# Optimization experiments

Measured on AMD Instinct MI355X. Metric: run time of the kernel, lower is better.

Reference implementation:

```python
import jax, jax.numpy as jnp
import numpy as np

EMBED_DIM = 512
HEADS = 8
ATTN_DIM = EMBED_DIM // HEADS
PF_DIM = 2048
B, L = 4, 2048
LN_EPS = 1e-5


def _linear(x, W, b):
    # nn.Linear: x @ W.T + b, W is [out, in]
    return jnp.einsum('bld,od->blo', x, W) + b


def _layer_norm(x, g, b):
    mu = jnp.mean(x, axis=-1, keepdims=True)
    var = jnp.mean(jnp.square(x - mu), axis=-1, keepdims=True)
    return (x - mu) * jax.lax.rsqrt(var + LN_EPS) * g + b


def _qkv(src, Wq, bq, Wk, bk, Wv, bv):
    def split(t):
        Bb, Ll, _ = t.shape
        return t.reshape(Bb, Ll, HEADS, ATTN_DIM).transpose(0, 2, 1, 3)  # [B,H,L,Dh]
    return (split(_linear(src, Wq, bq)),
            split(_linear(src, Wk, bk)),
            split(_linear(src, Wv, bv)))


def _attention(inp, Q, K1, K2, V1, V2, Wo, bo, ln_g, ln_b, W1, b1, W2, b2):
    # non-softmax linear attention: (Q K1^T) V1 + (Q K2^T) V2
    attn = (jnp.einsum('bhqk,bhkd->bhqd', jnp.einsum('bhqd,bhkd->bhqk', Q, K1), V1)
            + jnp.einsum('bhqk,bhkd->bhqd', jnp.einsum('bhqd,bhkd->bhqk', Q, K2), V2))
    Bb = Q.shape[0]
    attn = attn.transpose(0, 2, 1, 3).reshape(Bb, -1, HEADS * ATTN_DIM)  # [B,L,D]
    x = _linear(attn, Wo, bo)
    x = _layer_norm(inp + x, ln_g, ln_b)          # dropout p=0 (eval)
    ff = _linear(jax.nn.relu(_linear(x, W1, b1)), W2, b2)
    x = _layer_norm(x + ff, ln_g, ln_b)
    return x


def setup_inputs() -> dict:
    key = jax.random.key(0)
    ks = jax.random.split(key, 16)
    s = 0.02
    return {
        'question': jax.random.normal(ks[0], (B, L, EMBED_DIM), jnp.float32),
        'query': jax.random.normal(ks[1], (B, L, EMBED_DIM), jnp.float32),
        'Wq': jax.random.normal(ks[2], (EMBED_DIM, EMBED_DIM), jnp.float32) * s,
        'bq': jnp.zeros((EMBED_DIM,), jnp.float32),
        'Wk': jax.random.normal(ks[3], (EMBED_DIM, EMBED_DIM), jnp.float32) * s,
        'bk': jnp.zeros((EMBED_DIM,), jnp.float32),
        'Wv': jax.random.normal(ks[4], (EMBED_DIM, EMBED_DIM), jnp.float32) * s,
        'bv': jnp.zeros((EMBED_DIM,), jnp.float32),
        'Wo': jax.random.normal(ks[5], (EMBED_DIM, EMBED_DIM), jnp.float32) * s,
        'bo': jnp.zeros((EMBED_DIM,), jnp.float32),
        'ln_g': jnp.ones((EMBED_DIM,), jnp.float32),
        'ln_b': jnp.zeros((EMBED_DIM,), jnp.float32),
        'W1': jax.random.normal(ks[6], (PF_DIM, EMBED_DIM), jnp.float32) * s,
        'b1': jnp.zeros((PF_DIM,), jnp.float32),
        'W2': jax.random.normal(ks[7], (EMBED_DIM, PF_DIM), jnp.float32) * s,
        'b2': jnp.zeros((EMBED_DIM,), jnp.float32),
    }


def reference(question, query, Wq, bq, Wk, bk, Wv, bv, Wo, bo, ln_g, ln_b, W1, b1, W2, b2):
    Q1, K1, V1 = _qkv(question, Wq, bq, Wk, bk, Wv, bv)
    Q2, K2, V2 = _qkv(query, Wq, bq, Wk, bk, Wv, bv)
    question_attn = _attention(question, Q1, K1, K2, V1, V2, Wo, bo, ln_g, ln_b, W1, b1, W2, b2)
    query_attn = _attention(query, Q2, K2, K1, V2, V1, Wo, bo, ln_g, ln_b, W1, b1, W2, b2)
    return jnp.concatenate([question_attn, query_attn], axis=-1)
```

## Files before the change

### kernel.cpp

```cpp
#include <hip/hip_runtime.h>
#include <stdint.h>


#define Bq 4
#define Lq 2048
#define Dq 512
#define PFq 2048
#define Mrows 16384
#define MiBu 1048576ull
#define NSLICE 16

typedef __attribute__((ext_vector_type(8))) short frag_ab;
typedef __attribute__((ext_vector_type(4))) float frag_cd;
typedef __attribute__((ext_vector_type(8))) unsigned short ushort8v;

__device__ __forceinline__ unsigned short f2b(float f) {
    union { float f; uint32_t u; } x; x.f = f;
    uint32_t r = x.u + 0x7fffu + ((x.u >> 16) & 1u);
    return (unsigned short)(r >> 16);
}
__device__ __forceinline__ float b2f(unsigned short u) {
    union { uint32_t u; float f; } x; x.u = ((uint32_t)u) << 16;
    return x.f;
}

#define GLD16(g, l)                                                              \
    __builtin_amdgcn_global_load_lds(                                            \
        (const __attribute__((address_space(1))) void*)(const void*)(g),         \
        (__attribute__((address_space(3))) void*)(void*)(l), 16, 0, 0)

#define STG(BUFOFS, REGOFS, GB, ROWOFS, TILE, KS)                                \
    { GLD16((GB) + (size_t)(ROWOFS) * (KS) + (TILE) * 64,                        \
            Sh + (BUFOFS) + (REGOFS) + ld);                                      \
      GLD16((GB) + ((size_t)(ROWOFS) + 64) * (KS) + (TILE) * 64,                 \
            Sh + (BUFOFS) + (REGOFS) + ld + 4096); }

#define VMW(N) asm volatile("s_waitcnt vmcnt(" #N ")" ::: "memory")

#define PHASE(CB, M0, LOADB, STAGE_STMT, WAIT_STMT)                              \
    {                                                                            \
        frag_ab a00 = *(const frag_ab*)&Sh[(CB) + (wm + (M0)*16 + lr) * 64 + xo0];      \
        frag_ab a01 = *(const frag_ab*)&Sh[(CB) + (wm + (M0)*16 + lr) * 64 + xo1];      \
        frag_ab a10 = *(const frag_ab*)&Sh[(CB) + (wm + (M0)*16 + 16 + lr) * 64 + xo0]; \
        frag_ab a11 = *(const frag_ab*)&Sh[(CB) + (wm + (M0)*16 + 16 + lr) * 64 + xo1]; \
        if (LOADB) {                                                             \
            _Pragma("unroll")                                                    \
            for (int j = 0; j < 4; ++j) {                                        \
                bf[j][0] = *(const frag_ab*)&Sh[(CB) + 16384 + (wn + j*16 + lr)*64 + xo0]; \
                bf[j][1] = *(const frag_ab*)&Sh[(CB) + 16384 + (wn + j*16 + lr)*64 + xo1]; \
            }                                                                    \
        }                                                                        \
        STAGE_STMT;                                                              \
        WAIT_STMT;                                                               \
        __builtin_amdgcn_sched_barrier(0);                                       \
        __builtin_amdgcn_s_barrier();                                            \
        asm volatile("s_waitcnt lgkmcnt(0)" ::: "memory");                       \
        __builtin_amdgcn_sched_barrier(0);                                       \
        __builtin_amdgcn_s_setprio(1);                                           \
        _Pragma("unroll")                                                        \
        for (int j = 0; j < 4; ++j) {                                            \
            acc[(M0)][j]   = __builtin_amdgcn_mfma_f32_16x16x32_bf16(a00, bf[j][0], acc[(M0)][j], 0,0,0);   \
            acc[(M0)][j]   = __builtin_amdgcn_mfma_f32_16x16x32_bf16(a01, bf[j][1], acc[(M0)][j], 0,0,0);   \
            acc[(M0)+1][j] = __builtin_amdgcn_mfma_f32_16x16x32_bf16(a10, bf[j][0], acc[(M0)+1][j], 0,0,0); \
            acc[(M0)+1][j] = __builtin_amdgcn_mfma_f32_16x16x32_bf16(a11, bf[j][1], acc[(M0)+1][j], 0,0,0); \
        }                                                                        \
        __builtin_amdgcn_s_setprio(0);                                           \
        __builtin_amdgcn_sched_barrier(0);                                       \
        __builtin_amdgcn_s_barrier();                                            \
        __builtin_amdgcn_sched_barrier(0);                                       \
    }

__global__ __launch_bounds__(512, 2) void gemm_256(
    const unsigned short* __restrict__ A, const unsigned short* __restrict__ Wt,
    const float* __restrict__ bias, unsigned short* __restrict__ outB,
    int M, int N, int relu)
{
    __shared__ __align__(16) unsigned short Sh[65536];
    const int tid = threadIdx.x;
    const int lane = tid & 63;
    const int w = tid >> 6;
    const int wm = (w >> 2) * 128;
    const int wn = (w & 3) * 64;
    const int lr = lane & 15;
    const int quad = lane >> 4;
    const int xo0 = ((quad ^ (lr & 7)) << 3);
    const int xo1 = (((4 | quad) ^ (lr & 7)) << 3);

    const int b0 = blockIdx.x;
    const int xcd = b0 & 7, slot = b0 >> 3;
    const int mloc = (M >> 8) >> 3;
    const size_t bm = (size_t)(xcd * mloc + slot % mloc) * 256;
    const size_t bn = (size_t)(slot / mloc) * 256;

    const int ar = tid >> 3;
    const int sw = ((tid & 7) ^ (ar & 7)) << 3;
    const unsigned short* Ag = A  + (bm + ar) * (size_t)512 + sw;
    const unsigned short* Bg = Wt + (bn + ar) * (size_t)512 + sw;
    const int ld = tid * 8;

    frag_cd acc[8][4] = {};
    frag_ab bf[4][2];

    STG(0,     16384, Bg, 0,   0, 512);
    STG(0,     24576, Bg, 128, 0, 512);
    STG(0,     0,     Ag, 0,   0, 512);
    STG(0,     8192,  Ag, 128, 0, 512);
    STG(32768, 16384, Bg, 0,   1, 512);
    STG(32768, 24576, Bg, 128, 1, 512);
    VMW(4);
    __builtin_amdgcn_sched_barrier(0);
    __builtin_amdgcn_s_barrier();
    __builtin_amdgcn_sched_barrier(0);

    for (int I = 0; I < 3; ++I) {
        const int tb = 2 * I + 1, tc = 2 * I + 2, td = 2 * I + 3;
        PHASE(0,     0, 1, STG(32768, 0,     Ag, 0,   tb, 512), (void)0);
        PHASE(0,     2, 0, STG(32768, 8192,  Ag, 128, tb, 512), (void)0);
        PHASE(0,     4, 0, STG(0,     16384, Bg, 0,   tc, 512), (void)0);
        PHASE(0,     6, 0, STG(0,     24576, Bg, 128, tc, 512), VMW(4));
        PHASE(32768, 0, 1, STG(0,     0,     Ag, 0,   tc, 512), (void)0);
        PHASE(32768, 2, 0, STG(0,     8192,  Ag, 128, tc, 512), (void)0);
        PHASE(32768, 4, 0, STG(32768, 16384, Bg, 0,   td, 512), (void)0);
        PHASE(32768, 6, 0, STG(32768, 24576, Bg, 128, td, 512), VMW(4));
    }
    PHASE(0,     0, 1, STG(32768, 0,    Ag, 0,   7, 512), (void)0);
    PHASE(0,     2, 0, STG(32768, 8192, Ag, 128, 7, 512), (void)0);
    PHASE(0,     4, 0, (void)0, (void)0);
    PHASE(0,     6, 0, (void)0, VMW(0));
    PHASE(32768, 0, 1, (void)0, (void)0);
    PHASE(32768, 2, 0, (void)0, (void)0);
    PHASE(32768, 4, 0, (void)0, (void)0);
    PHASE(32768, 6, 0, (void)0, (void)0);

    float bv[4];
#pragma unroll
    for (int j = 0; j < 4; ++j) bv[j] = bias[(int)bn + wn + j * 16 + lr];
    unsigned short* Cs = Sh + w * 8192;
#pragma unroll
    for (int m = 0; m < 8; ++m)
#pragma unroll
        for (int j = 0; j < 4; ++j)
#pragma unroll
            for (int r = 0; r < 4; ++r) {
                float v = acc[m][j][r] + bv[j];
                if (relu) v = fmaxf(v, 0.f);
                Cs[(m * 16 + quad * 4 + r) * 64 + j * 16 + lr] = f2b(v);
            }
    const int rl = lane >> 3, c8 = (lane & 7) * 8;
#pragma unroll
    for (int k = 0; k < 16; ++k) {
        const int row = rl + k * 8;
        ushort8v val = *(const ushort8v*)&Cs[row * 64 + c8];
        *(ushort8v*)(outB + (size_t)(bm + wm + row) * N + bn + wn + c8) = val;
    }
}

__global__ __launch_bounds__(512, 2) void gemm_n128(
    const unsigned short* __restrict__ A, const unsigned short* __restrict__ Wt,
    const float* __restrict__ bias,
    const float* __restrict__ resA, const float* __restrict__ resB,
    unsigned short* __restrict__ outB, int N, int K, int mode)
{
    __shared__ __align__(16) unsigned short Sh[49152];
    const int tid = threadIdx.x;
    const int lane = tid & 63;
    const int w = tid >> 6;
    const int wm = (w >> 1) * 64;
    const int wn = (w & 1) * 64;
    const int lr = lane & 15;
    const int quad = lane >> 4;
    const int xo0 = ((quad ^ (lr & 7)) << 3);
    const int xo1 = (((4 | quad) ^ (lr & 7)) << 3);

    const int b0 = blockIdx.x;
    const int xcd = b0 & 7, slot = b0 >> 3;
    const size_t bm = (size_t)(xcd * 8 + (slot & 7)) * 256;
    const size_t bn = (size_t)(slot >> 3) * 128;

    const int ar = tid >> 3;
    const int sw = ((tid & 7) ^ (ar & 7)) << 3;
    const unsigned short* Ag = A  + (bm + ar) * (size_t)K + sw;
    const unsigned short* Bg = Wt + (bn + ar) * (size_t)K + sw;
    const int ld = tid * 8;

    frag_cd acc[4][4] = {};
    frag_ab bf[4][2];

    STG(0,     16384, Bg, 0,   0, K);
    STG(0,     0,     Ag, 0,   0, K);
    STG(0,     8192,  Ag, 128, 0, K);
    STG(24576, 16384, Bg, 0,   1, K);
    VMW(2);
    __builtin_amdgcn_sched_barrier(0);
    __builtin_amdgcn_s_barrier();
    __builtin_amdgcn_sched_barrier(0);

    const int nIter = K >> 7;
    for (int I = 0; I < nIter - 1; ++I) {
        const int tb = 2 * I + 1, tc = 2 * I + 2, td = 2 * I + 3;
        PHASE(0,     0, 1, { STG(24576, 0, Ag, 0, tb, K); STG(24576, 8192, Ag, 128, tb, K); }, (void)0);
        PHASE(0,     2, 0, STG(0, 16384, Bg, 0, tc, K), VMW(2));
        PHASE(24576, 0, 1, { STG(0, 0, Ag, 0, tc, K); STG(0, 8192, Ag, 128, tc, K); }, (void)0);
        PHASE(24576, 2, 0, STG(24576, 16384, Bg, 0, td, K), VMW(2));
    }
    {
        const int tb = (K >> 6) - 1;
        PHASE(0,     0, 1, { STG(24576, 0, Ag, 0, tb, K); STG(24576, 8192, Ag, 128, tb, K); }, (void)0);
        PHASE(0,     2, 0, (void)0, VMW(0));
        PHASE(24576, 0, 1, (void)0, (void)0);
        PHASE(24576, 2, 0, (void)0, (void)0);
    }

    float bv[4];
#pragma unroll
    for (int j = 0; j < 4; ++j) bv[j] = bias[(int)bn + wn + j * 16 + lr];
    unsigned short* Cs = Sh + w * 4096;
#pragma unroll
    for (int m = 0; m < 4; ++m)
#pragma unroll
        for (int j = 0; j < 4; ++j)
#pragma unroll
            for (int r = 0; r < 4; ++r)
                Cs[(m * 16 + quad * 4 + r) * 64 + j * 16 + lr] = f2b(acc[m][j][r] + bv[j]);
    const int rl = lane >> 3, c8 = (lane & 7) * 8;
#pragma unroll
    for (int k = 0; k < 8; ++k) {
        const int row = rl + k * 8;
        const int grow = (int)bm + wm + row;
        const size_t idx = (size_t)grow * N + bn + wn + c8;
        ushort8v val = *(const ushort8v*)&Cs[row * 64 + c8];
        if (mode == 0) {
            *(ushort8v*)(outB + idx) = val;
            continue;
        }
        float vv[8];
#pragma unroll
        for (int t = 0; t < 8; ++t) vv[t] = b2f(val[t]);
        if (mode == 1) {
            const float* rp = (grow < 8192) ? resA + idx : resB + idx - (size_t)8192 * N;
            float4 ra = *(const float4*)(rp);
            float4 rb = *(const float4*)(rp + 4);
            vv[0] += ra.x; vv[1] += ra.y; vv[2] += ra.z; vv[3] += ra.w;
            vv[4] += rb.x; vv[5] += rb.y; vv[6] += rb.z; vv[7] += rb.w;
        } else {
            ushort8v old = *(const ushort8v*)(outB + idx);
#pragma unroll
            for (int t = 0; t < 8; ++t) vv[t] += b2f(old[t]);
        }
        ushort8v o;
#pragma unroll
        for (int t = 0; t < 8; ++t) o[t] = f2b(vv[t]);
        *(ushort8v*)(outB + idx) = o;
    }
}

__global__ __launch_bounds__(256) void convert_all(
    const float* __restrict__ Wq, const float* __restrict__ Wk,
    const float* __restrict__ Wv, const float* __restrict__ Wo,
    const float* __restrict__ W1, const float* __restrict__ W2,
    const float* __restrict__ question, const float* __restrict__ query,
    const float* __restrict__ bqp, const float* __restrict__ bkp,
    const float* __restrict__ bvp,
    unsigned short* __restrict__ Wqkvb, unsigned short* __restrict__ Wob,
    unsigned short* __restrict__ W1b, unsigned short* __restrict__ W2b,
    unsigned short* __restrict__ Xb, float* __restrict__ bqkv)
{
    const int b = blockIdx.x;
    const float* src; unsigned short* dst; size_t off;
    if (b < 256)        { src = Wq; dst = Wqkvb;          off = (size_t)b * 1024; }
    else if (b < 512)   { src = Wk; dst = Wqkvb + 262144; off = (size_t)(b - 256) * 1024; }
    else if (b < 768)   { src = Wv; dst = Wqkvb + 524288; off = (size_t)(b - 512) * 1024; }
    else if (b < 1024)  { src = Wo; dst = Wob;            off = (size_t)(b - 768) * 1024; }
    else if (b < 2048)  { src = W1; dst = W1b;            off = (size_t)(b - 1024) * 1024; }
    else if (b < 3072)  { src = W2; dst = W2b;            off = (size_t)(b - 2048) * 1024; }
    else if (b < 7168)  { src = question; dst = Xb;       off = (size_t)(b - 3072) * 1024; }
    else if (b < 11264) { src = query; dst = Xb + 4194304; off = (size_t)(b - 7168) * 1024; }
    else {
        const int n = (b - 11264) * 256 + threadIdx.x;
        bqkv[n] = (n < 512) ? bqp[n] : (n < 1024) ? bkp[n - 512] : bvp[n - 1024];
        return;
    }
    const size_t idx = off + threadIdx.x * 4;
    float4 v = *(const float4*)(src + idx);
    ushort4 o;
    o.x = f2b(v.x); o.y = f2b(v.y); o.z = f2b(v.z); o.w = f2b(v.w);
    *(ushort4*)(dst + idx) = o;
}

__global__ __launch_bounds__(256) void s_kernel(
    const unsigned short* __restrict__ QKV, float* __restrict__ Spart)
{
    const int bh = blockIdx.x;
    const int sl = blockIdx.y;
    const int b = bh >> 3, h = bh & 7;
    const int pass = sl >> 3;
    const int l0 = (sl & 7) * 256;
    __shared__ float Ks[64][64];
    __shared__ float Vs[64][64];
    const int tid = threadIdx.x;
    const int tx = tid & 15, ty = tid >> 4;
    const int srow = tid >> 3;
    const int scol = (tid & 7) * 8;
    const size_t rowbase = (size_t)pass * 8192 + (size_t)b * Lq + l0;

    float acc[4][4] = {};

    for (int t0 = 0; t0 < 256; t0 += 64) {
        const unsigned short* kp0 = QKV + (rowbase + t0 + srow) * 1536 + 512 + h * 64 + scol;
        const unsigned short* kp1 = kp0 + (size_t)32 * 1536;
        ushort8v k0 = *(const ushort8v*)kp0;
        ushort8v v0 = *(const ushort8v*)(kp0 + 512);
        ushort8v k1 = *(const ushort8v*)kp1;
        ushort8v v1 = *(const ushort8v*)(kp1 + 512);
        __syncthreads();
#pragma unroll
        for (int e = 0; e < 8; ++e) {
            Ks[srow][scol + e]      = b2f(k0[e]);
            Vs[srow][scol + e]      = b2f(v0[e]);
            Ks[srow + 32][scol + e] = b2f(k1[e]);
            Vs[srow + 32][scol + e] = b2f(v1[e]);
        }
        __syncthreads();
#pragma unroll 4
        for (int rr = 0; rr < 64; ++rr) {
            const float4 kf = *(const float4*)&Ks[rr][ty * 4];
            const float4 vf = *(const float4*)&Vs[rr][tx * 4];
            acc[0][0] = fmaf(kf.x, vf.x, acc[0][0]);
            acc[0][1] = fmaf(kf.x, vf.y, acc[0][1]);
            acc[0][2] = fmaf(kf.x, vf.z, acc[0][2]);
            acc[0][3] = fmaf(kf.x, vf.w, acc[0][3]);
            acc[1][0] = fmaf(kf.y, vf.x, acc[1][0]);
            acc[1][1] = fmaf(kf.y, vf.y, acc[1][1]);
            acc[1][2] = fmaf(kf.y, vf.z, acc[1][2]);
            acc[1][3] = fmaf(kf.y, vf.w, acc[1][3]);
            acc[2][0] = fmaf(kf.z, vf.x, acc[2][0]);
            acc[2][1] = fmaf(kf.z, vf.y, acc[2][1]);
            acc[2][2] = fmaf(kf.z, vf.z, acc[2][2]);
            acc[2][3] = fmaf(kf.z, vf.w, acc[2][3]);
            acc[3][0] = fmaf(kf.w, vf.x, acc[3][0]);
            acc[3][1] = fmaf(kf.w, vf.y, acc[3][1]);
            acc[3][2] = fmaf(kf.w, vf.z, acc[3][2]);
            acc[3][3] = fmaf(kf.w, vf.w, acc[3][3]);
        }
    }

    float* Sp = Spart + ((size_t)bh * NSLICE + sl) * 4096;
#pragma unroll
    for (int i = 0; i < 4; ++i) {
        float4 o = make_float4(acc[i][0], acc[i][1], acc[i][2], acc[i][3]);
        *(float4*)(Sp + (ty * 4 + i) * 64 + tx * 4) = o;
    }
}

__global__ __launch_bounds__(256) void sbt_convert(
    const float* __restrict__ Spart, unsigned short* __restrict__ Sbt)
{
    const int bh = blockIdx.x;
    const int uo = blockIdx.y;
    const float* Sp = Spart + (size_t)bh * (NSLICE * 4096);
    unsigned short* Dp = Sbt + (size_t)bh * 4096;
    const int t = threadIdx.x;
#pragma unroll
    for (int u = 0; u < 4; ++u) {
        const int d = (uo * 4 + u) * 256 + t;
        float v = 0.f;
#pragma unroll
        for (int s = 0; s < NSLICE; ++s) v += Sp[(size_t)s * 4096 + d];
        const int row = d >> 6, col = d & 63;
        Dp[(row >> 5) * 2048 + col * 32 + (row & 31)] = f2b(v);
    }
}

__global__ __launch_bounds__(256) void attn_mfma(
    const unsigned short* __restrict__ QKV, const unsigned short* __restrict__ Sbt,
    unsigned short* __restrict__ Ob)
{
    __shared__ __align__(16) unsigned short Sh[2 * 128 * 32 + 2 * 64 * 32];
    unsigned short* At = Sh;
    unsigned short* Bt = Sh + 2 * 128 * 32;
    const int h = blockIdx.x;
    const int rbase = blockIdx.y * 128;
    const int b = (rbase >> 11) & 3;
    const int bh = b * 8 + h;
    const int tid = threadIdx.x;
    const int lane = tid & 63;
    const int w = tid >> 6;
    const int lr = lane & 15;
    const int quad = lane >> 4;

    {
        const int rloc = tid >> 2, c8 = (tid & 3) * 8;
#pragma unroll
        for (int it = 0; it < 4; ++it) {
            const int kk = it & 1, rh = it >> 1;
            const unsigned short* g = QKV +
                ((size_t)rbase + rh * 64 + rloc) * 1536 + h * 64 + kk * 32 + c8;
            GLD16(g, At + kk * 4096 + rh * 2048 + w * 512);
        }
        const unsigned short* Sg = Sbt + (size_t)bh * 4096 + tid * 8;
#pragma unroll
        for (int bi = 0; bi < 2; ++bi)
            GLD16(Sg + bi * 2048, Bt + bi * 2048 + w * 512);
    }
    __syncthreads();

    frag_cd acc[2][4] = {};
#pragma unroll
    for (int kk = 0; kk < 2; ++kk) {
        frag_ab a[2], bfr[4];
#pragma unroll
        for (int i = 0; i < 2; ++i)
            a[i] = *(const frag_ab*)&At[kk * 4096 + (w * 32 + i * 16 + lr) * 32 + quad * 8];
#pragma unroll
        for (int j = 0; j < 4; ++j)
            bfr[j] = *(const frag_ab*)&Bt[kk * 2048 + (j * 16 + lr) * 32 + quad * 8];
#pragma unroll
        for (int i = 0; i < 2; ++i)
#pragma unroll
            for (int j = 0; j < 4; ++j)
                acc[i][j] = __builtin_amdgcn_mfma_f32_16x16x32_bf16(a[i], bfr[j], acc[i][j], 0, 0, 0);
    }

    __syncthreads();
    unsigned short* Cs = Sh + w * 2048;
#pragma unroll
    for (int i = 0; i < 2; ++i)
#pragma unroll
        for (int j = 0; j < 4; ++j)
#pragma unroll
            for (int r = 0; r < 4; ++r)
                Cs[(i * 16 + quad * 4 + r) * 64 + j * 16 + lr] = f2b(acc[i][j][r]);
    const int rl = lane >> 3;
    const int c8o = (lane & 7) * 8;
#pragma unroll
    for (int k = 0; k < 4; ++k) {
        const int row = rl + k * 8;
        ushort8v val = *(const ushort8v*)&Cs[row * 64 + c8o];
        *(ushort8v*)(Ob + (size_t)(rbase + w * 32 + row) * 512 + h * 64 + c8o) = val;
    }
}

__global__ __launch_bounds__(256) void ln_b16_inplace(
    unsigned short* __restrict__ Y, const float* __restrict__ g,
    const float* __restrict__ bta)
{
    __shared__ float part[8];
    const int row = blockIdx.x;
    const int t = threadIdx.x;
    const int w = t >> 6;
    unsigned short* yr = Y + (size_t)row * Dq;
    const float v0 = b2f(yr[t]), v1 = b2f(yr[t + 256]);
    float s = v0 + v1;
#pragma unroll
    for (int off = 32; off; off >>= 1) s += __shfl_xor(s, off, 64);
    if ((t & 63) == 0) part[w] = s;
    __syncthreads();
    const float mean = (part[0] + part[1] + part[2] + part[3]) * (1.f / Dq);
    const float d0 = v0 - mean, d1 = v1 - mean;
    float q = d0 * d0 + d1 * d1;
#pragma unroll
    for (int off = 32; off; off >>= 1) q += __shfl_xor(q, off, 64);
    if ((t & 63) == 0) part[4 + w] = q;
    __syncthreads();
    const float rstd = rsqrtf((part[4] + part[5] + part[6] + part[7]) * (1.f / Dq) + 1e-5f);
    yr[t] = f2b(d0 * rstd * g[t] + bta[t]);
    yr[t + 256] = f2b(d1 * rstd * g[t + 256] + bta[t + 256]);
}

__global__ __launch_bounds__(256) void ln_b16_out(
    const unsigned short* __restrict__ Y, const float* __restrict__ g,
    const float* __restrict__ bta, float* __restrict__ out)
{
    __shared__ float part[8];
    const int row = blockIdx.x;
    const int t = threadIdx.x;
    const int w = t >> 6;
    const unsigned short* yr = Y + (size_t)row * Dq;
    const float v0 = b2f(yr[t]), v1 = b2f(yr[t + 256]);
    float s = v0 + v1;
#pragma unroll
    for (int off = 32; off; off >>= 1) s += __shfl_xor(s, off, 64);
    if ((t & 63) == 0) part[w] = s;
    __syncthreads();
    const float mean = (part[0] + part[1] + part[2] + part[3]) * (1.f / Dq);
    const float d0 = v0 - mean, d1 = v1 - mean;
    float q = d0 * d0 + d1 * d1;
#pragma unroll
    for (int off = 32; off; off >>= 1) q += __shfl_xor(q, off, 64);
    if ((t & 63) == 0) part[4 + w] = q;
    __syncthreads();
    const float rstd = rsqrtf((part[4] + part[5] + part[6] + part[7]) * (1.f / Dq) + 1e-5f);
    const int half = row >> 13, br = row & 8191;
    float* orow = out + (size_t)br * 1024 + half * 512;
    orow[t] = d0 * rstd * g[t] + bta[t];
    orow[t + 256] = d1 * rstd * g[t + 256] + bta[t + 256];
}

extern "C" void kernel_launch(void* const* d_in, const int* in_sizes, int n_in,
                              void* d_out, int out_size, void* d_ws, size_t ws_size,
                              hipStream_t stream)
{
    const float* question = (const float*)d_in[0];
    const float* query    = (const float*)d_in[1];
    const float* Wq = (const float*)d_in[2];  const float* bqp = (const float*)d_in[3];
    const float* Wk = (const float*)d_in[4];  const float* bkp = (const float*)d_in[5];
    const float* Wv = (const float*)d_in[6];  const float* bvp = (const float*)d_in[7];
    const float* Wo = (const float*)d_in[8];  const float* bo  = (const float*)d_in[9];
    const float* ln_g = (const float*)d_in[10]; const float* ln_b = (const float*)d_in[11];
    const float* W1 = (const float*)d_in[12]; const float* b1 = (const float*)d_in[13];
    const float* W2 = (const float*)d_in[14]; const float* b2 = (const float*)d_in[15];
    float* out = (float*)d_out;
    char* ws = (char*)d_ws;

    unsigned short* QKVb  = (unsigned short*)(ws);
    unsigned short* attnb = (unsigned short*)(ws + 48 * MiBu);
    float* Spart          = (float*)(ws + 48 * MiBu);
    unsigned short* Xb    = (unsigned short*)(ws + 64 * MiBu);
    unsigned short* xbuf  = (unsigned short*)(ws + 64 * MiBu);
    unsigned short* hb    = (unsigned short*)(ws);
    char* wp = ws + 80 * MiBu + 524288;
    unsigned short* Wqkvb = (unsigned short*)wp;  wp += 1536 * 512 * 2;
    unsigned short* Wob   = (unsigned short*)wp;  wp += 512 * 512 * 2;
    unsigned short* W1b   = (unsigned short*)wp;  wp += 2048 * 512 * 2;
    unsigned short* W2b   = (unsigned short*)wp;  wp += 512 * 2048 * 2;
    unsigned short* Sbt   = (unsigned short*)wp;  wp += 32 * 4096 * 2;
    float* bqkv           = (float*)wp;

    dim3 blk(256);

    convert_all<<<11270, blk, 0, stream>>>(Wq, Wk, Wv, Wo, W1, W2, question, query,
                                           bqp, bkp, bvp,
                                           Wqkvb, Wob, W1b, W2b, Xb, bqkv);

    gemm_n128<<<dim3(768), dim3(512), 0, stream>>>(Xb, Wqkvb, bqkv,
                                                   nullptr, nullptr, QKVb,
                                                   1536, 512, 0);

    s_kernel<<<dim3(32, NSLICE), blk, 0, stream>>>(QKVb, Spart);
    sbt_convert<<<dim3(32, 4), blk, 0, stream>>>(Spart, Sbt);
    attn_mfma<<<dim3(8, 128), blk, 0, stream>>>(QKVb, Sbt, attnb);

    gemm_n128<<<dim3(256), dim3(512), 0, stream>>>(attnb, Wob, bo,
                                                   question, query, xbuf,
                                                   512, 512, 1);

    ln_b16_inplace<<<Mrows, blk, 0, stream>>>(xbuf, ln_g, ln_b);

    gemm_256<<<dim3(512), dim3(512), 0, stream>>>(xbuf, W1b, b1, hb,
                                                  Mrows, PFq, 1);

    gemm_n128<<<dim3(256), dim3(512), 0, stream>>>(hb, W2b, b2,
                                                   nullptr, nullptr, xbuf,
                                                   512, 2048, 2);

    ln_b16_out<<<Mrows, blk, 0, stream>>>(xbuf, ln_g, ln_b, out);
}
```

Before: 301.0 us.

## Unify GEMMs into triple-buffered 256x128 kernel with a deeper prefetch pipeline

Replaces the 256x256 FFN1 GEMM and the double-buffered 256x128 GEMM with one triple-buffered 256x128 kernel that keeps two K-tiles in flight. It generalises the M mapping and adds a ReLU flag, so FFN1 now runs on 1024 smaller tiles. The deeper prefetch is meant to hide global-load latency. In exchange it uses more LDS (144KB per block), which may reduce occupancy, and FFN1 loses the larger tile's data reuse.

```diff
diff --git a/kernel.cpp b/kernel.cpp
--- a/kernel.cpp
+++ b/kernel.cpp
@@ -30,9 +30,9 @@
         (__attribute__((address_space(3))) void*)(void*)(l), 16, 0, 0)
 
 #define STG(BUFOFS, REGOFS, GB, ROWOFS, TILE, KS)                                \
-    { GLD16((GB) + (size_t)(ROWOFS) * (KS) + (TILE) * 64,                        \
+    { GLD16((GB) + (size_t)(ROWOFS) * (KS) + (size_t)(TILE) * 64,                \
             Sh + (BUFOFS) + (REGOFS) + ld);                                      \
-      GLD16((GB) + ((size_t)(ROWOFS) + 64) * (KS) + (TILE) * 64,                 \
+      GLD16((GB) + ((size_t)(ROWOFS) + 64) * (KS) + (size_t)(TILE) * 64,         \
             Sh + (BUFOFS) + (REGOFS) + ld + 4096); }
 
 #define VMW(N) asm volatile("s_waitcnt vmcnt(" #N ")" ::: "memory")
@@ -70,98 +70,13 @@
         __builtin_amdgcn_sched_barrier(0);                                       \
     }
 
-__global__ __launch_bounds__(512, 2) void gemm_256(
-    const unsigned short* __restrict__ A, const unsigned short* __restrict__ Wt,
-    const float* __restrict__ bias, unsigned short* __restrict__ outB,
-    int M, int N, int relu)
-{
-    __shared__ __align__(16) unsigned short Sh[65536];
-    const int tid = threadIdx.x;
-    const int lane = tid & 63;
-    const int w = tid >> 6;
-    const int wm = (w >> 2) * 128;
-    const int wn = (w & 3) * 64;
-    const int lr = lane & 15;
-    const int quad = lane >> 4;
-    const int xo0 = ((quad ^ (lr & 7)) << 3);
-    const int xo1 = (((4 | quad) ^ (lr & 7)) << 3);
-
-    const int b0 = blockIdx.x;
-    const int xcd = b0 & 7, slot = b0 >> 3;
-    const int mloc = (M >> 8) >> 3;
-    const size_t bm = (size_t)(xcd * mloc + slot % mloc) * 256;
-    const size_t bn = (size_t)(slot / mloc) * 256;
-
-    const int ar = tid >> 3;
-    const int sw = ((tid & 7) ^ (ar & 7)) << 3;
-    const unsigned short* Ag = A  + (bm + ar) * (size_t)512 + sw;
-    const unsigned short* Bg = Wt + (bn + ar) * (size_t)512 + sw;
-    const int ld = tid * 8;
-
-    frag_cd acc[8][4] = {};
-    frag_ab bf[4][2];
-
-    STG(0,     16384, Bg, 0,   0, 512);
-    STG(0,     24576, Bg, 128, 0, 512);
-    STG(0,     0,     Ag, 0,   0, 512);
-    STG(0,     8192,  Ag, 128, 0, 512);
-    STG(32768, 16384, Bg, 0,   1, 512);
-    STG(32768, 24576, Bg, 128, 1, 512);
-    VMW(4);
-    __builtin_amdgcn_sched_barrier(0);
-    __builtin_amdgcn_s_barrier();
-    __builtin_amdgcn_sched_barrier(0);
-
-    for (int I = 0; I < 3; ++I) {
-        const int tb = 2 * I + 1, tc = 2 * I + 2, td = 2 * I + 3;
-        PHASE(0,     0, 1, STG(32768, 0,     Ag, 0,   tb, 512), (void)0);
-        PHASE(0,     2, 0, STG(32768, 8192,  Ag, 128, tb, 512), (void)0);
-        PHASE(0,     4, 0, STG(0,     16384, Bg, 0,   tc, 512), (void)0);
-        PHASE(0,     6, 0, STG(0,     24576, Bg, 128, tc, 512), VMW(4));
-        PHASE(32768, 0, 1, STG(0,     0,     Ag, 0,   tc, 512), (void)0);
-        PHASE(32768, 2, 0, STG(0,     8192,  Ag, 128, tc, 512), (void)0);
-        PHASE(32768, 4, 0, STG(32768, 16384, Bg, 0,   td, 512), (void)0);
-        PHASE(32768, 6, 0, STG(32768, 24576, Bg, 128, td, 512), VMW(4));
-    }
-    PHASE(0,     0, 1, STG(32768, 0,    Ag, 0,   7, 512), (void)0);
-    PHASE(0,     2, 0, STG(32768, 8192, Ag, 128, 7, 512), (void)0);
-    PHASE(0,     4, 0, (void)0, (void)0);
-    PHASE(0,     6, 0, (void)0, VMW(0));
-    PHASE(32768, 0, 1, (void)0, (void)0);
-    PHASE(32768, 2, 0, (void)0, (void)0);
-    PHASE(32768, 4, 0, (void)0, (void)0);
-    PHASE(32768, 6, 0, (void)0, (void)0);
-
-    float bv[4];
-#pragma unroll
-    for (int j = 0; j < 4; ++j) bv[j] = bias[(int)bn + wn + j * 16 + lr];
-    unsigned short* Cs = Sh + w * 8192;
-#pragma unroll
-    for (int m = 0; m < 8; ++m)
-#pragma unroll
-        for (int j = 0; j < 4; ++j)
-#pragma unroll
-            for (int r = 0; r < 4; ++r) {
-                float v = acc[m][j][r] + bv[j];
-                if (relu) v = fmaxf(v, 0.f);
-                Cs[(m * 16 + quad * 4 + r) * 64 + j * 16 + lr] = f2b(v);
-            }
-    const int rl = lane >> 3, c8 = (lane & 7) * 8;
-#pragma unroll
-    for (int k = 0; k < 16; ++k) {
-        const int row = rl + k * 8;
-        ushort8v val = *(const ushort8v*)&Cs[row * 64 + c8];
-        *(ushort8v*)(outB + (size_t)(bm + wm + row) * N + bn + wn + c8) = val;
-    }
-}
-
-__global__ __launch_bounds__(512, 2) void gemm_n128(
+__global__ __launch_bounds__(512, 2) void gemm_t3(
     const unsigned short* __restrict__ A, const unsigned short* __restrict__ Wt,
     const float* __restrict__ bias,
     const float* __restrict__ resA, const float* __restrict__ resB,
-    unsigned short* __restrict__ outB, int N, int K, int mode)
-{
-    __shared__ __align__(16) unsigned short Sh[49152];
+    unsigned short* __restrict__ outB, int M, int N, int K, int mode, int relu)
+{
+    __shared__ __align__(16) unsigned short Sh[73728];
     const int tid = threadIdx.x;
     const int lane = tid & 63;
     const int w = tid >> 6;
@@ -174,8 +89,9 @@
 
     const int b0 = blockIdx.x;
     const int xcd = b0 & 7, slot = b0 >> 3;
-    const size_t bm = (size_t)(xcd * 8 + (slot & 7)) * 256;
-    const size_t bn = (size_t)(slot >> 3) * 128;
+    const int mloc = (M >> 8) >> 3;
+    const size_t bm = (size_t)(xcd * mloc + slot % mloc) * 256;
+    const size_t bn = (size_t)(slot / mloc) * 128;
 
     const int ar = tid >> 3;
     const int sw = ((tid & 7) ^ (ar & 7)) << 3;
@@ -186,29 +102,32 @@
     frag_cd acc[4][4] = {};
     frag_ab bf[4][2];
 
-    STG(0,     16384, Bg, 0,   0, K);
+    const int nt = K >> 6;
+
     STG(0,     0,     Ag, 0,   0, K);
     STG(0,     8192,  Ag, 128, 0, K);
+    STG(0,     16384, Bg, 0,   0, K);
+    STG(24576, 0,     Ag, 0,   1, K);
+    STG(24576, 8192,  Ag, 128, 1, K);
     STG(24576, 16384, Bg, 0,   1, K);
-    VMW(2);
+    VMW(6);
     __builtin_amdgcn_sched_barrier(0);
     __builtin_amdgcn_s_barrier();
     __builtin_amdgcn_sched_barrier(0);
 
-    const int nIter = K >> 7;
-    for (int I = 0; I < nIter - 1; ++I) {
-        const int tb = 2 * I + 1, tc = 2 * I + 2, td = 2 * I + 3;
-        PHASE(0,     0, 1, { STG(24576, 0, Ag, 0, tb, K); STG(24576, 8192, Ag, 128, tb, K); }, (void)0);
-        PHASE(0,     2, 0, STG(0, 16384, Bg, 0, tc, K), VMW(2));
-        PHASE(24576, 0, 1, { STG(0, 0, Ag, 0, tc, K); STG(0, 8192, Ag, 128, tc, K); }, (void)0);
-        PHASE(24576, 2, 0, STG(24576, 16384, Bg, 0, td, K), VMW(2));
-    }
-    {
-        const int tb = (K >> 6) - 1;
-        PHASE(0,     0, 1, { STG(24576, 0, Ag, 0, tb, K); STG(24576, 8192, Ag, 128, tb, K); }, (void)0);
-        PHASE(0,     2, 0, (void)0, VMW(0));
-        PHASE(24576, 0, 1, (void)0, (void)0);
-        PHASE(24576, 2, 0, (void)0, (void)0);
+    int cbuf = 0;
+    for (int t = 0; t < nt; ++t) {
+        const int sbuf = (cbuf == 0) ? 49152 : cbuf - 24576;
+        const int ts = t + 2;
+        const bool st = (ts < nt);
+        const bool more = (t + 1 < nt);
+        PHASE(cbuf, 0, 1,
+              { if (st) { STG(sbuf, 0, Ag, 0, ts, K); STG(sbuf, 8192, Ag, 128, ts, K); } },
+              (void)0);
+        PHASE(cbuf, 2, 0,
+              { if (st) { STG(sbuf, 16384, Bg, 0, ts, K); } },
+              { if (st) { VMW(6); } else if (more) { VMW(0); } });
+        cbuf = (cbuf == 49152) ? 0 : cbuf + 24576;
     }
 
     float bv[4];
@@ -220,8 +139,11 @@
 #pragma unroll
         for (int j = 0; j < 4; ++j)
 #pragma unroll
-            for (int r = 0; r < 4; ++r)
-                Cs[(m * 16 + quad * 4 + r) * 64 + j * 16 + lr] = f2b(acc[m][j][r] + bv[j]);
+            for (int r = 0; r < 4; ++r) {
+                float v = acc[m][j][r] + bv[j];
+                if (relu) v = fmaxf(v, 0.f);
+                Cs[(m * 16 + quad * 4 + r) * 64 + j * 16 + lr] = f2b(v);
+            }
     const int rl = lane >> 3, c8 = (lane & 7) * 8;
 #pragma unroll
     for (int k = 0; k < 8; ++k) {
@@ -235,7 +157,7 @@
         }
         float vv[8];
 #pragma unroll
-        for (int t = 0; t < 8; ++t) vv[t] = b2f(val[t]);
+        for (int t2 = 0; t2 < 8; ++t2) vv[t2] = b2f(val[t2]);
         if (mode == 1) {
             const float* rp = (grow < 8192) ? resA + idx : resB + idx - (size_t)8192 * N;
             float4 ra = *(const float4*)(rp);
@@ -245,11 +167,11 @@
         } else {
             ushort8v old = *(const ushort8v*)(outB + idx);
 #pragma unroll
-            for (int t = 0; t < 8; ++t) vv[t] += b2f(old[t]);
+            for (int t2 = 0; t2 < 8; ++t2) vv[t2] += b2f(old[t2]);
         }
         ushort8v o;
 #pragma unroll
-        for (int t = 0; t < 8; ++t) o[t] = f2b(vv[t]);
+        for (int t2 = 0; t2 < 8; ++t2) o[t2] = f2b(vv[t2]);
         *(ushort8v*)(outB + idx) = o;
     }
 }
@@ -532,26 +454,27 @@
                                            bqp, bkp, bvp,
                                            Wqkvb, Wob, W1b, W2b, Xb, bqkv);
 
-    gemm_n128<<<dim3(768), dim3(512), 0, stream>>>(Xb, Wqkvb, bqkv,
-                                                   nullptr, nullptr, QKVb,
-                                                   1536, 512, 0);
+    gemm_t3<<<dim3(768), dim3(512), 0, stream>>>(Xb, Wqkvb, bqkv,
+                                                 nullptr, nullptr, QKVb,
+                                                 Mrows, 1536, 512, 0, 0);
 
     s_kernel<<<dim3(32, NSLICE), blk, 0, stream>>>(QKVb, Spart);
     sbt_convert<<<dim3(32, 4), blk, 0, stream>>>(Spart, Sbt);
     attn_mfma<<<dim3(8, 128), blk, 0, stream>>>(QKVb, Sbt, attnb);
 
-    gemm_n128<<<dim3(256), dim3(512), 0, stream>>>(attnb, Wob, bo,
-                                                   question, query, xbuf,
-                                                   512, 512, 1);
+    gemm_t3<<<dim3(256), dim3(512), 0, stream>>>(attnb, Wob, bo,
+                                                 question, query, xbuf,
+                                                 Mrows, 512, 512, 1, 0);
 
     ln_b16_inplace<<<Mrows, blk, 0, stream>>>(xbuf, ln_g, ln_b);
 
-    gemm_256<<<dim3(512), dim3(512), 0, stream>>>(xbuf, W1b, b1, hb,
-                                                  Mrows, PFq, 1);
-
-    gemm_n128<<<dim3(256), dim3(512), 0, stream>>>(hb, W2b, b2,
-                                                   nullptr, nullptr, xbuf,
-                                                   512, 2048, 2);
+    gemm_t3<<<dim3(1024), dim3(512), 0, stream>>>(xbuf, W1b, b1,
+                                                  nullptr, nullptr, hb,
+                                                  Mrows, PFq, 512, 0, 1);
+
+    gemm_t3<<<dim3(256), dim3(512), 0, stream>>>(hb, W2b, b2,
+                                                 nullptr, nullptr, xbuf,
+                                                 Mrows, 512, 2048, 2, 0);
 
     ln_b16_out<<<Mrows, blk, 0, stream>>>(xbuf, ln_g, ln_b, out);
 }
```

Measured after the change: 321.5 us. 1.07x slower.

## Fold Q projection and output projection into per-batch fused weight

Applied to the files above, without the earlier changes.

Because the attention has no softmax, out = X·Wq^T·S·Wo^T per batch, so the Q projection is dropped. A small per-batch matrix U = Wq^T S is built and fused with Wo into one 512x512 weight per batch, with a matching bias. The separate attention kernel and the Q slice of the QKV GEMM go away, and the output projection GEMM reads the raw input directly with per-batch weights. The cost is a few tiny extra kernels, an atomicAdd bias reduction, and extra bf16 rounding in the fused weights.

```diff
diff --git a/kernel.cpp b/kernel.cpp
--- a/kernel.cpp
+++ b/kernel.cpp
@@ -30,9 +30,9 @@
         (__attribute__((address_space(3))) void*)(void*)(l), 16, 0, 0)
 
 #define STG(BUFOFS, REGOFS, GB, ROWOFS, TILE, KS)                                \
-    { GLD16((GB) + (size_t)(ROWOFS) * (KS) + (TILE) * 64,                        \
+    { GLD16((GB) + (size_t)(ROWOFS) * (KS) + (size_t)(TILE) * 64,                \
             Sh + (BUFOFS) + (REGOFS) + ld);                                      \
-      GLD16((GB) + ((size_t)(ROWOFS) + 64) * (KS) + (TILE) * 64,                 \
+      GLD16((GB) + ((size_t)(ROWOFS) + 64) * (KS) + (size_t)(TILE) * 64,         \
             Sh + (BUFOFS) + (REGOFS) + ld + 4096); }
 
 #define VMW(N) asm volatile("s_waitcnt vmcnt(" #N ")" ::: "memory")
@@ -159,7 +159,7 @@
     const unsigned short* __restrict__ A, const unsigned short* __restrict__ Wt,
     const float* __restrict__ bias,
     const float* __restrict__ resA, const float* __restrict__ resB,
-    unsigned short* __restrict__ outB, int N, int K, int mode)
+    unsigned short* __restrict__ outB, int N, int K, int mode, int perb)
 {
     __shared__ __align__(16) unsigned short Sh[49152];
     const int tid = threadIdx.x;
@@ -177,6 +177,12 @@
     const size_t bm = (size_t)(xcd * 8 + (slot & 7)) * 256;
     const size_t bn = (size_t)(slot >> 3) * 128;
 
+    if (perb) {
+        const int bsel = ((int)(bm >> 11)) & 3;
+        Wt += (size_t)bsel << 18;
+        bias += bsel << 9;
+    }
+
     const int ar = tid >> 3;
     const int sw = ((tid & 7) ^ (ar & 7)) << 3;
     const unsigned short* Ag = A  + (bm + ar) * (size_t)K + sw;
@@ -235,7 +241,7 @@
         }
         float vv[8];
 #pragma unroll
-        for (int t = 0; t < 8; ++t) vv[t] = b2f(val[t]);
+        for (int t2 = 0; t2 < 8; ++t2) vv[t2] = b2f(val[t2]);
         if (mode == 1) {
             const float* rp = (grow < 8192) ? resA + idx : resB + idx - (size_t)8192 * N;
             float4 ra = *(const float4*)(rp);
@@ -245,12 +251,80 @@
         } else {
             ushort8v old = *(const ushort8v*)(outB + idx);
 #pragma unroll
-            for (int t = 0; t < 8; ++t) vv[t] += b2f(old[t]);
+            for (int t2 = 0; t2 < 8; ++t2) vv[t2] += b2f(old[t2]);
         }
         ushort8v o;
 #pragma unroll
-        for (int t = 0; t < 8; ++t) o[t] = f2b(vv[t]);
+        for (int t2 = 0; t2 < 8; ++t2) o[t2] = f2b(vv[t2]);
         *(ushort8v*)(outB + idx) = o;
+    }
+}
+
+__global__ __launch_bounds__(256) void gemm_fuse(
+    const unsigned short* __restrict__ Wob, const unsigned short* __restrict__ UT,
+    unsigned short* __restrict__ Wfin)
+{
+    __shared__ __align__(16) unsigned short Sh[2 * 128 * 64];
+    unsigned short* At = Sh;
+    unsigned short* Bt = Sh + 128 * 64;
+    const int tid = threadIdx.x;
+    const int lane = tid & 63;
+    const int w = tid >> 6;
+    const int wm = (w >> 1) * 64, wn = (w & 1) * 64;
+    const int lr = lane & 15;
+    const int quad = lane >> 4;
+    const int bb = blockIdx.z;
+    const size_t bm = (size_t)blockIdx.x * 128, bn = (size_t)blockIdx.y * 128;
+
+    frag_cd acc[4][4] = {};
+    const int ar = tid >> 3;
+    const int acs = (((tid & 7) ^ (ar & 7)) << 3);
+    const unsigned short* Ag = Wob + (bm + ar) * 512 + acs;
+    const unsigned short* Bg = UT + ((size_t)bb << 18) + (bn + ar) * 512 + acs;
+    unsigned short* Asd = At + w * 512;
+    unsigned short* Bsd = Bt + w * 512;
+
+    for (int k0 = 0; k0 < 512; k0 += 64) {
+        __syncthreads();
+#pragma unroll
+        for (int i = 0; i < 4; ++i) {
+            GLD16(Ag + (size_t)(32 * i) * 512 + k0, Asd + i * 2048);
+            GLD16(Bg + (size_t)(32 * i) * 512 + k0, Bsd + i * 2048);
+        }
+        __syncthreads();
+#pragma unroll
+        for (int kk = 0; kk < 2; ++kk) {
+            frag_ab a[4], b[4];
+#pragma unroll
+            for (int i = 0; i < 4; ++i)
+                a[i] = *(const frag_ab*)&At[(wm + i * 16 + lr) * 64 +
+                                            ((((kk << 2) | quad) ^ (lr & 7)) << 3)];
+#pragma unroll
+            for (int j = 0; j < 4; ++j)
+                b[j] = *(const frag_ab*)&Bt[(wn + j * 16 + lr) * 64 +
+                                            ((((kk << 2) | quad) ^ (lr & 7)) << 3)];
+#pragma unroll
+            for (int i = 0; i < 4; ++i)
+#pragma unroll
+                for (int j = 0; j < 4; ++j)
+                    acc[i][j] = __builtin_amdgcn_mfma_f32_16x16x32_bf16(a[i], b[j], acc[i][j], 0, 0, 0);
+        }
+    }
+    __syncthreads();
+    unsigned short* Cs = Sh + w * 4096;
+#pragma unroll
+    for (int j = 0; j < 4; ++j)
+#pragma unroll
+        for (int i = 0; i < 4; ++i)
+#pragma unroll
+            for (int r = 0; r < 4; ++r)
+                Cs[(i * 16 + quad * 4 + r) * 64 + j * 16 + lr] = f2b(acc[i][j][r]);
+    const int rl = lane >> 3, c8 = (lane & 7) * 8;
+#pragma unroll
+    for (int k = 0; k < 8; ++k) {
+        const int row = rl + k * 8;
+        ushort8v val = *(const ushort8v*)&Cs[row * 64 + c8];
+        *(ushort8v*)(Wfin + ((size_t)bb << 18) + (bm + wm + row) * 512 + bn + wn + c8) = val;
     }
 }
 
@@ -260,10 +334,11 @@
     const float* __restrict__ W1, const float* __restrict__ W2,
     const float* __restrict__ question, const float* __restrict__ query,
     const float* __restrict__ bqp, const float* __restrict__ bkp,
-    const float* __restrict__ bvp,
+    const float* __restrict__ bvp, const float* __restrict__ bo,
     unsigned short* __restrict__ Wqkvb, unsigned short* __restrict__ Wob,
     unsigned short* __restrict__ W1b, unsigned short* __restrict__ W2b,
-    unsigned short* __restrict__ Xb, float* __restrict__ bqkv)
+    unsigned short* __restrict__ Xb, float* __restrict__ bqkv,
+    float* __restrict__ biasO)
 {
     const int b = blockIdx.x;
     const float* src; unsigned short* dst; size_t off;
@@ -275,9 +350,13 @@
     else if (b < 3072)  { src = W2; dst = W2b;            off = (size_t)(b - 2048) * 1024; }
     else if (b < 7168)  { src = question; dst = Xb;       off = (size_t)(b - 3072) * 1024; }
     else if (b < 11264) { src = query; dst = Xb + 4194304; off = (size_t)(b - 7168) * 1024; }
-    else {
+    else if (b < 11270) {
         const int n = (b - 11264) * 256 + threadIdx.x;
         bqkv[n] = (n < 512) ? bqp[n] : (n < 1024) ? bkp[n - 512] : bvp[n - 1024];
+        return;
+    } else {
+        const int n = (b - 11270) * 256 + threadIdx.x;
+        biasO[n] = bo[n & 511];
         return;
     }
     const size_t idx = off + threadIdx.x * 4;
@@ -306,8 +385,8 @@
     float acc[4][4] = {};
 
     for (int t0 = 0; t0 < 256; t0 += 64) {
-        const unsigned short* kp0 = QKV + (rowbase + t0 + srow) * 1536 + 512 + h * 64 + scol;
-        const unsigned short* kp1 = kp0 + (size_t)32 * 1536;
+        const unsigned short* kp0 = QKV + (rowbase + t0 + srow) * 1024 + h * 64 + scol;
+        const unsigned short* kp1 = kp0 + (size_t)32 * 1024;
         ushort8v k0 = *(const ushort8v*)kp0;
         ushort8v v0 = *(const ushort8v*)(kp0 + 512);
         ushort8v k1 = *(const ushort8v*)kp1;
@@ -352,13 +431,12 @@
     }
 }
 
-__global__ __launch_bounds__(256) void sbt_convert(
-    const float* __restrict__ Spart, unsigned short* __restrict__ Sbt)
-{
-    const int bh = blockIdx.x;
-    const int uo = blockIdx.y;
+__global__ __launch_bounds__(256) void s_reduce(
+    const float* __restrict__ Spart, float* __restrict__ Sred)
+{
+    const int bh = blockIdx.x, uo = blockIdx.y;
     const float* Sp = Spart + (size_t)bh * (NSLICE * 4096);
-    unsigned short* Dp = Sbt + (size_t)bh * 4096;
+    float* Dp = Sred + (size_t)bh * 4096;
     const int t = threadIdx.x;
 #pragma unroll
     for (int u = 0; u < 4; ++u) {
@@ -366,78 +444,53 @@
         float v = 0.f;
 #pragma unroll
         for (int s = 0; s < NSLICE; ++s) v += Sp[(size_t)s * 4096 + d];
-        const int row = d >> 6, col = d & 63;
-        Dp[(row >> 5) * 2048 + col * 32 + (row & 31)] = f2b(v);
-    }
-}
-
-__global__ __launch_bounds__(256) void attn_mfma(
-    const unsigned short* __restrict__ QKV, const unsigned short* __restrict__ Sbt,
-    unsigned short* __restrict__ Ob)
-{
-    __shared__ __align__(16) unsigned short Sh[2 * 128 * 32 + 2 * 64 * 32];
-    unsigned short* At = Sh;
-    unsigned short* Bt = Sh + 2 * 128 * 32;
-    const int h = blockIdx.x;
-    const int rbase = blockIdx.y * 128;
-    const int b = (rbase >> 11) & 3;
-    const int bh = b * 8 + h;
-    const int tid = threadIdx.x;
-    const int lane = tid & 63;
-    const int w = tid >> 6;
-    const int lr = lane & 15;
-    const int quad = lane >> 4;
-
-    {
-        const int rloc = tid >> 2, c8 = (tid & 3) * 8;
-#pragma unroll
-        for (int it = 0; it < 4; ++it) {
-            const int kk = it & 1, rh = it >> 1;
-            const unsigned short* g = QKV +
-                ((size_t)rbase + rh * 64 + rloc) * 1536 + h * 64 + kk * 32 + c8;
-            GLD16(g, At + kk * 4096 + rh * 2048 + w * 512);
-        }
-        const unsigned short* Sg = Sbt + (size_t)bh * 4096 + tid * 8;
-#pragma unroll
-        for (int bi = 0; bi < 2; ++bi)
-            GLD16(Sg + bi * 2048, Bt + bi * 2048 + w * 512);
-    }
+        Dp[d] = v;
+    }
+}
+
+__global__ __launch_bounds__(512) void u_kernel(
+    const float* __restrict__ Sred, const unsigned short* __restrict__ Wqb,
+    const unsigned short* __restrict__ Wob, const float* __restrict__ bq,
+    unsigned short* __restrict__ UT, float* __restrict__ biasO)
+{
+    const int bh = blockIdx.x, jh = blockIdx.y;
+    const int b = bh >> 3, h = bh & 7;
+    __shared__ float Sf[4096];
+    __shared__ float rsh[32];
+    const int t = threadIdx.x;
+#pragma unroll
+    for (int e = 0; e < 8; ++e)
+        Sf[e * 512 + t] = Sred[(size_t)bh * 4096 + e * 512 + t];
     __syncthreads();
 
-    frag_cd acc[2][4] = {};
-#pragma unroll
-    for (int kk = 0; kk < 2; ++kk) {
-        frag_ab a[2], bfr[4];
-#pragma unroll
-        for (int i = 0; i < 2; ++i)
-            a[i] = *(const frag_ab*)&At[kk * 4096 + (w * 32 + i * 16 + lr) * 32 + quad * 8];
-#pragma unroll
-        for (int j = 0; j < 4; ++j)
-            bfr[j] = *(const frag_ab*)&Bt[kk * 2048 + (j * 16 + lr) * 32 + quad * 8];
-#pragma unroll
-        for (int i = 0; i < 2; ++i)
-#pragma unroll
-            for (int j = 0; j < 4; ++j)
-                acc[i][j] = __builtin_amdgcn_mfma_f32_16x16x32_bf16(a[i], bfr[j], acc[i][j], 0, 0, 0);
-    }
-
+    const int j0 = jh * 32;
+    float T[32] = {};
+    for (int k = 0; k < 64; ++k) {
+        const float wq = b2f(Wqb[(h * 64 + k) * 512 + t]);
+#pragma unroll
+        for (int j = 0; j < 32; ++j)
+            T[j] = fmaf(wq, Sf[k * 64 + j0 + j], T[j]);
+    }
+    unsigned short* up = UT + ((size_t)(b * 512 + t)) * 512 + h * 64 + j0;
+#pragma unroll
+    for (int g = 0; g < 4; ++g) {
+        ushort8v o;
+#pragma unroll
+        for (int e = 0; e < 8; ++e) o[e] = f2b(T[g * 8 + e]);
+        *(ushort8v*)(up + g * 8) = o;
+    }
+
+    if (t < 32) {
+        float r = 0.f;
+        for (int k = 0; k < 64; ++k) r += bq[h * 64 + k] * Sf[k * 64 + j0 + t];
+        rsh[t] = r;
+    }
     __syncthreads();
-    unsigned short* Cs = Sh + w * 2048;
-#pragma unroll
-    for (int i = 0; i < 2; ++i)
-#pragma unroll
-        for (int j = 0; j < 4; ++j)
-#pragma unroll
-            for (int r = 0; r < 4; ++r)
-                Cs[(i * 16 + quad * 4 + r) * 64 + j * 16 + lr] = f2b(acc[i][j][r]);
-    const int rl = lane >> 3;
-    const int c8o = (lane & 7) * 8;
-#pragma unroll
-    for (int k = 0; k < 4; ++k) {
-        const int row = rl + k * 8;
-        ushort8v val = *(const ushort8v*)&Cs[row * 64 + c8o];
-        *(ushort8v*)(Ob + (size_t)(rbase + w * 32 + row) * 512 + h * 64 + c8o) = val;
-    }
+    float c = 0.f;
+#pragma unroll
+    for (int j = 0; j < 32; ++j)
+        c += rsh[j] * b2f(Wob[(size_t)t * 512 + h * 64 + j0 + j]);
+    atomicAdd(&biasO[b * 512 + t], c);
 }
 
 __global__ __launch_bounds__(256) void ln_b16_inplace(
@@ -512,37 +565,40 @@
     float* out = (float*)d_out;
     char* ws = (char*)d_ws;
 
-    unsigned short* QKVb  = (unsigned short*)(ws);
-    unsigned short* attnb = (unsigned short*)(ws + 48 * MiBu);
-    float* Spart          = (float*)(ws + 48 * MiBu);
-    unsigned short* Xb    = (unsigned short*)(ws + 64 * MiBu);
-    unsigned short* xbuf  = (unsigned short*)(ws + 64 * MiBu);
-    unsigned short* hb    = (unsigned short*)(ws);
-    char* wp = ws + 80 * MiBu + 524288;
+    unsigned short* QKVb = (unsigned short*)(ws);
+    unsigned short* UT   = (unsigned short*)(ws + 32 * MiBu);
+    unsigned short* Wfin = (unsigned short*)(ws + 34 * MiBu);
+    float* Sred          = (float*)(ws + 36 * MiBu);
+    float* Spart         = (float*)(ws + 40 * MiBu);
+    unsigned short* hb   = (unsigned short*)(ws);
+    unsigned short* xbuf = (unsigned short*)(ws + 64 * MiBu);
+    unsigned short* Xb   = (unsigned short*)d_out;
+    char* wp = ws + 80 * MiBu;
     unsigned short* Wqkvb = (unsigned short*)wp;  wp += 1536 * 512 * 2;
     unsigned short* Wob   = (unsigned short*)wp;  wp += 512 * 512 * 2;
     unsigned short* W1b   = (unsigned short*)wp;  wp += 2048 * 512 * 2;
     unsigned short* W2b   = (unsigned short*)wp;  wp += 512 * 2048 * 2;
-    unsigned short* Sbt   = (unsigned short*)wp;  wp += 32 * 4096 * 2;
+    float* biasO          = (float*)wp;           wp += 4 * 512 * 4;
     float* bqkv           = (float*)wp;
 
     dim3 blk(256);
 
-    convert_all<<<11270, blk, 0, stream>>>(Wq, Wk, Wv, Wo, W1, W2, question, query,
-                                           bqp, bkp, bvp,
-                                           Wqkvb, Wob, W1b, W2b, Xb, bqkv);
-
-    gemm_n128<<<dim3(768), dim3(512), 0, stream>>>(Xb, Wqkvb, bqkv,
+    convert_all<<<11278, blk, 0, stream>>>(Wq, Wk, Wv, Wo, W1, W2, question, query,
+                                           bqp, bkp, bvp, bo,
+                                           Wqkvb, Wob, W1b, W2b, Xb, bqkv, biasO);
+
+    gemm_n128<<<dim3(512), dim3(512), 0, stream>>>(Xb, Wqkvb + 262144, bqkv + 512,
                                                    nullptr, nullptr, QKVb,
-                                                   1536, 512, 0);
+                                                   1024, 512, 0, 0);
 
     s_kernel<<<dim3(32, NSLICE), blk, 0, stream>>>(QKVb, Spart);
-    sbt_convert<<<dim3(32, 4), blk, 0, stream>>>(Spart, Sbt);
-    attn_mfma<<<dim3(8, 128), blk, 0, stream>>>(QKVb, Sbt, attnb);
-
-    gemm_n128<<<dim3(256), dim3(512), 0, stream>>>(attnb, Wob, bo,
+    s_reduce<<<dim3(32, 4), blk, 0, stream>>>(Spart, Sred);
+    u_kernel<<<dim3(32, 2), dim3(512), 0, stream>>>(Sred, Wqkvb, Wob, bqkv, UT, biasO);
+    gemm_fuse<<<dim3(4, 4, 4), blk, 0, stream>>>(Wob, UT, Wfin);
+
+    gemm_n128<<<dim3(256), dim3(512), 0, stream>>>(Xb, Wfin, biasO,
                                                    question, query, xbuf,
-                                                   512, 512, 1);
+                                                   512, 512, 1, 1);
 
     ln_b16_inplace<<<Mrows, blk, 0, stream>>>(xbuf, ln_g, ln_b);
 
@@ -551,7 +607,7 @@
 
     gemm_n128<<<dim3(256), dim3(512), 0, stream>>>(hb, W2b, b2,
                                                    nullptr, nullptr, xbuf,
-                                                   512, 2048, 2);
+                                                   512, 2048, 2, 0);
 
     ln_b16_out<<<Mrows, blk, 0, stream>>>(xbuf, ln_g, ln_b, out);
 }
```

After: 311.8 us. +3.6%, slower.
